# Optimization experiments

Measured on AMD Instinct MI355X. Metric: run time of the kernel, lower is better.

The kernel has to match this reference:

```python
import jax, jax.numpy as jnp
import numpy as np


def setup_inputs() -> dict:
    key = jax.random.key(0)
    k1, k2, k3, k4 = jax.random.split(key, 4)
    H = W = D = 192
    I = jax.random.normal(k1, (1, 1, H, W, D), dtype=jnp.float32)
    dx_t = jax.random.normal(k2, (1, H, W, D), dtype=jnp.float32)
    dy_t = jax.random.normal(k3, (1, H, W, D), dtype=jnp.float32)
    dz_t = jax.random.normal(k4, (1, H, W, D), dtype=jnp.float32)
    return {"I": I, "dx_t": dx_t, "dy_t": dy_t, "dz_t": dz_t}


def reference(I, dx_t, dy_t, dz_t):
    # Trilinear warp, faithful to the torch module (valid for batch=1).
    B, C, H, W, D = I.shape
    # Identity meshgrid: x varies along width (axis 1), y along height (axis 0),
    # z along depth (axis 2) -- matches the numpy construction in __init__.
    x_mesh = jnp.arange(W, dtype=jnp.float32)[None, :, None]
    y_mesh = jnp.arange(H, dtype=jnp.float32)[:, None, None]
    z_mesh = jnp.arange(D, dtype=jnp.float32)[None, None, :]
    # +1 accounts for the zero-padding of I by 1 voxel on every side.
    x = dx_t[0] + x_mesh + 1.0  # [H,W,D]
    y = dy_t[0] + y_mesh + 1.0
    z = dz_t[0] + z_mesh + 1.0

    Ip = jnp.pad(I[0], ((0, 0), (1, 1), (1, 1), (1, 1)))  # [C,H+2,W+2,D+2]
    Hp, Wp, Dp = H + 2, W + 2, D + 2

    fx = jnp.floor(x).astype(jnp.int32)
    fy = jnp.floor(y).astype(jnp.int32)
    fz = jnp.floor(z).astype(jnp.int32)
    x0 = jnp.clip(fx, 0, Wp - 1); x1 = jnp.clip(fx + 1, 0, Wp - 1)
    y0 = jnp.clip(fy, 0, Hp - 1); y1 = jnp.clip(fy + 1, 0, Hp - 1)
    z0 = jnp.clip(fz, 0, Dp - 1); z1 = jnp.clip(fz + 1, 0, Dp - 1)

    # Fractional weights computed from the *clamped* upper corner (faithful).
    dx = x1.astype(jnp.float32) - x
    dy = y1.astype(jnp.float32) - y
    dz = z1.astype(jnp.float32) - z

    # Gather 8 corners: padded volume layout is [C, y, x, z].
    Ia = Ip[:, y0, x0, z0]
    Ib = Ip[:, y1, x0, z0]
    Ic = Ip[:, y0, x1, z0]
    Id = Ip[:, y1, x1, z0]
    Ie = Ip[:, y0, x0, z1]
    If = Ip[:, y1, x0, z1]
    Ig = Ip[:, y0, x1, z1]
    Ih = Ip[:, y1, x1, z1]

    wa = dz * dx * dy
    wb = dz * dx * (1 - dy)
    wc = dz * (1 - dx) * dy
    wd = dz * (1 - dx) * (1 - dy)
    we = (1 - dz) * dx * dy
    wf = (1 - dz) * dx * (1 - dy)
    wg = (1 - dz) * (1 - dx) * dy
    wh = (1 - dz) * (1 - dx) * (1 - dy)

    out = (wa * Ia + wb * Ib + wc * Ic + wd * Id
           + we * Ie + wf * If + wg * Ig + wh * Ih)  # [C,H,W,D]
    return out[None]  # [1,C,H,W,D]
```

## Files before the change

### kernel.cpp

```cpp
#include <hip/hip_runtime.h>

constexpr int H = 192, W = 192, D = 192;
constexpr int BH = 8, BW = 8, BZ = 16;
constexpr int TY = 16, TX = 16, TZ = 24;
constexpr int WD = W * D;

__device__ __forceinline__ float ref_voxel(const float* __restrict__ I,
                                           float x, float y, float zf)
{
    int fx = (int)floorf(x), fy = (int)floorf(y), fz = (int)floorf(zf);
    int x0 = min(max(fx, 0), W + 1), x1 = min(max(fx + 1, 0), W + 1);
    int y0 = min(max(fy, 0), H + 1), y1 = min(max(fy + 1, 0), H + 1);
    int zp0 = min(max(fz, 0), D + 1), zp1 = min(max(fz + 1, 0), D + 1);
    float dx = (float)x1 - x, dy = (float)y1 - y, dz = (float)zp1 - zf;
    int xi0 = x0 - 1, xi1 = x1 - 1, yi0 = y0 - 1, yi1 = y1 - 1;
    int zi = zp0 - 1, zj = zp1 - 1;
    float ax0 = ((unsigned)xi0 < (unsigned)W) ? dx       : 0.f;
    float ax1 = ((unsigned)xi1 < (unsigned)W) ? 1.f - dx : 0.f;
    float ay0 = ((unsigned)yi0 < (unsigned)H) ? dy       : 0.f;
    float ay1 = ((unsigned)yi1 < (unsigned)H) ? 1.f - dy : 0.f;
    float az0 = ((unsigned)zi  < (unsigned)D) ? dz       : 0.f;
    float az1 = ((unsigned)zj  < (unsigned)D) ? 1.f - dz : 0.f;
    int xc0 = min(max(xi0, 0), W - 1), xc1 = min(max(xi1, 0), W - 1);
    int yc0 = min(max(yi0, 0), H - 1), yc1 = min(max(yi1, 0), H - 1);
    int zc0 = min(max(zi, 0), D - 1),  zc1 = min(max(zj, 0), D - 1);
    const float* r00 = I + (yc0 * W + xc0) * D;
    const float* r01 = I + (yc0 * W + xc1) * D;
    const float* r10 = I + (yc1 * W + xc0) * D;
    const float* r11 = I + (yc1 * W + xc1) * D;
    float s00 = az0 * r00[zc0] + az1 * r00[zc1];
    float s01 = az0 * r01[zc0] + az1 * r01[zc1];
    float s10 = az0 * r10[zc0] + az1 * r10[zc1];
    float s11 = az0 * r11[zc0] + az1 * r11[zc1];
    return ay0 * (ax0 * s00 + ax1 * s01) + ay1 * (ax0 * s10 + ax1 * s11);
}

__global__ __launch_bounds__(256) void st_tile(
    const float* __restrict__ I,
    const float* __restrict__ dxt,
    const float* __restrict__ dyt,
    const float* __restrict__ dzt,
    float* __restrict__ out)
{
    __shared__ float tile[TY * TX * TZ];

    const int tid = threadIdx.x;
    const int bx = blockIdx.x, by = blockIdx.y, bz = blockIdx.z;
    const int w0 = bx * BW, h0 = by * BH, z0 = bz * BZ;
    const int xg0 = w0 - 4, yg0 = h0 - 4, zg0 = z0 - 4;

    const int zq = tid & 3, wl = (tid >> 2) & 7, hl = tid >> 5;
    const int h = h0 + hl, w = w0 + wl, z = z0 + zq * 4;
    const int t4 = (h * W + w) * (D / 4) + (z >> 2);

    float4 vx = reinterpret_cast<const float4*>(dxt)[t4];
    float4 vy = reinterpret_cast<const float4*>(dyt)[t4];
    float4 vz = reinterpret_cast<const float4*>(dzt)[t4];

    const bool interior = (bx >= 1) & (bx <= 22) & (by >= 1) & (by <= 22)
                        & (bz >= 1) & (bz <= 10);

    float rxj[4] = {vx.x, vx.y, vx.z, vx.w};
    float ryj[4] = {vy.x, vy.y, vy.z, vy.w};
    float rzj[4] = {vz.x, vz.y, vz.z, vz.w};
    float ro[4];

    if (interior) {
        {
            const float* p0 = I + ((yg0 * W + xg0) * D + zg0);
            float4 vals[6];
            #pragma unroll
            for (int it = 0; it < 6; ++it) {
                int g = it * 256 + tid;
                int row = g / 6, c = g - row * 6;
                int ry = row >> 4, rx = row & 15;
                vals[it] = *reinterpret_cast<const float4*>(p0 + (ry * W + rx) * D + c * 4);
            }
            #pragma unroll
            for (int it = 0; it < 6; ++it) {
                *reinterpret_cast<float4*>(
                    reinterpret_cast<char*>(tile) + (size_t)(it * 4096 + tid * 16)) = vals[it];
            }
        }
        __syncthreads();

        #pragma unroll
        for (int j = 0; j < 4; ++j) {
            float ux = rxj[j] + (float)(wl + 4);
            float uy = ryj[j] + (float)(hl + 4);
            float uz = rzj[j] + (float)(zq * 4 + j + 4);

            float fxf = floorf(ux), fyf = floorf(uy), fzf = floorf(uz);
            int lx0 = (int)fxf, ly0 = (int)fyf, lz0 = (int)fzf;
            float tx = ux - fxf, ty = uy - fyf, tz = uz - fzf;

            bool ok = ((unsigned)lx0 <= (unsigned)(TX - 2))
                    & ((unsigned)ly0 <= (unsigned)(TY - 2))
                    & ((unsigned)lz0 <= (unsigned)(TZ - 2));

            if (__builtin_expect(ok, 1)) {
                int base = (ly0 * TX + lx0) * TZ + lz0;
                float a0 = tile[base],        a1 = tile[base + 1];
                float b0 = tile[base + TZ],   b1 = tile[base + TZ + 1];
                float c0 = tile[base + TX*TZ],     c1 = tile[base + TX*TZ + 1];
                float d0 = tile[base + TX*TZ+TZ],  d1 = tile[base + TX*TZ+TZ + 1];
                float wz0 = 1.f - tz, wz1 = tz;
                float wx0 = 1.f - tx, wx1 = tx;
                float wy0 = 1.f - ty, wy1 = ty;
                float s00 = wz0 * a0 + wz1 * a1;
                float s01 = wz0 * b0 + wz1 * b1;
                float s10 = wz0 * c0 + wz1 * c1;
                float s11 = wz0 * d0 + wz1 * d1;
                ro[j] = wy0 * (wx0 * s00 + wx1 * s01) + wy1 * (wx0 * s10 + wx1 * s11);
            } else {
                float x = rxj[j] + (float)(w + 1);
                float y = ryj[j] + (float)(h + 1);
                float zf = rzj[j] + (float)(z + j + 1);
                ro[j] = ref_voxel(I, x, y, zf);
            }
        }
    } else {
        {
            float4 vals[6];
            #pragma unroll
            for (int it = 0; it < 6; ++it) {
                int g = it * 256 + tid;
                int row = g / 6, c = g - row * 6;
                int ry = row >> 4, rx = row & 15;
                int gy = min(max(yg0 + ry, 0), H - 1);
                int gx = min(max(xg0 + rx, 0), W - 1);
                const float* rp = I + (gy * W + gx) * D;
                int zb = zg0 + c * 4;
                vals[it] = make_float4(rp[min(max(zb + 0, 0), D - 1)],
                                       rp[min(max(zb + 1, 0), D - 1)],
                                       rp[min(max(zb + 2, 0), D - 1)],
                                       rp[min(max(zb + 3, 0), D - 1)]);
            }
            #pragma unroll
            for (int it = 0; it < 6; ++it) {
                *reinterpret_cast<float4*>(
                    reinterpret_cast<char*>(tile) + (size_t)(it * 4096 + tid * 16)) = vals[it];
            }
        }
        __syncthreads();

        #pragma unroll
        for (int j = 0; j < 4; ++j) {
            float x = rxj[j] + (float)(w + 1);
            float y = ryj[j] + (float)(h + 1);
            float zf = rzj[j] + (float)(z + j + 1);

            int fx = (int)floorf(x), fy = (int)floorf(y), fz = (int)floorf(zf);
            int x0 = min(max(fx, 0), W + 1), x1 = min(max(fx + 1, 0), W + 1);
            int y0 = min(max(fy, 0), H + 1), y1 = min(max(fy + 1, 0), H + 1);
            int zp0 = min(max(fz, 0), D + 1), zp1 = min(max(fz + 1, 0), D + 1);

            float dx = (float)x1 - x, dy = (float)y1 - y, dz = (float)zp1 - zf;

            int xi0 = x0 - 1, xi1 = x1 - 1, yi0 = y0 - 1, yi1 = y1 - 1;
            int zi = zp0 - 1, zj2 = zp1 - 1;

            float ax0 = ((unsigned)xi0 < (unsigned)W) ? dx       : 0.f;
            float ax1 = ((unsigned)xi1 < (unsigned)W) ? 1.f - dx : 0.f;
            float ay0 = ((unsigned)yi0 < (unsigned)H) ? dy       : 0.f;
            float ay1 = ((unsigned)yi1 < (unsigned)H) ? 1.f - dy : 0.f;
            float az0 = ((unsigned)zi  < (unsigned)D) ? dz       : 0.f;
            float az1 = ((unsigned)zj2 < (unsigned)D) ? 1.f - dz : 0.f;

            int xc0 = min(max(xi0, 0), W - 1), xc1 = min(max(xi1, 0), W - 1);
            int yc0 = min(max(yi0, 0), H - 1), yc1 = min(max(yi1, 0), H - 1);
            int zc  = min(max(zi, 0), D - 2);

            bool zlo = (zi <= D - 2);
            bool zhi = (zi >= 0);

            int lx0 = xc0 - xg0, lx1 = xc1 - xg0;
            int ly0 = yc0 - yg0, ly1 = yc1 - yg0;
            int lz  = zc - zg0;

            bool ok = ((unsigned)lx0 <= (unsigned)(TX - 1))
                    & ((unsigned)lx1 <= (unsigned)(TX - 1))
                    & ((unsigned)ly0 <= (unsigned)(TY - 1))
                    & ((unsigned)ly1 <= (unsigned)(TY - 1))
                    & ((unsigned)lz  <= (unsigned)(TZ - 2));

            if (__builtin_expect(ok, 1)) {
                int b00 = (ly0 * TX + lx0) * TZ + lz;
                int b01 = (ly0 * TX + lx1) * TZ + lz;
                int b10 = (ly1 * TX + lx0) * TZ + lz;
                int b11 = (ly1 * TX + lx1) * TZ + lz;
                float a0 = tile[b00], a1 = tile[b00 + 1];
                float b0 = tile[b01], b1 = tile[b01 + 1];
                float c0 = tile[b10], c1 = tile[b10 + 1];
                float d0 = tile[b11], d1 = tile[b11 + 1];
                float v000 = zlo ? a0 : a1, v001 = zhi ? a1 : a0;
                float v010 = zlo ? b0 : b1, v011 = zhi ? b1 : b0;
                float v100 = zlo ? c0 : c1, v101 = zhi ? c1 : c0;
                float v110 = zlo ? d0 : d1, v111 = zhi ? d1 : d0;
                float s00 = az0 * v000 + az1 * v001;
                float s01 = az0 * v010 + az1 * v011;
                float s10 = az0 * v100 + az1 * v101;
                float s11 = az0 * v110 + az1 * v111;
                ro[j] = ay0 * (ax0 * s00 + ax1 * s01)
                      + ay1 * (ax0 * s10 + ax1 * s11);
            } else {
                ro[j] = ref_voxel(I, x, y, zf);
            }
        }
    }

    reinterpret_cast<float4*>(out)[t4] = make_float4(ro[0], ro[1], ro[2], ro[3]);
}

extern "C" void kernel_launch(void* const* d_in, const int* in_sizes, int n_in,
                              void* d_out, int out_size, void* d_ws, size_t ws_size,
                              hipStream_t stream) {
    const float* I   = (const float*)d_in[0];
    const float* dxt = (const float*)d_in[1];
    const float* dyt = (const float*)d_in[2];
    const float* dzt = (const float*)d_in[3];
    float* out = (float*)d_out;

    dim3 grid(W / BW, H / BH, D / BZ);
    hipLaunchKernelGGL(st_tile, grid, dim3(256), 0, stream,
                       I, dxt, dyt, dzt, out);
}
```

Measured before the change: 53.85 us.

## Enlarge warp tiles and stage the volume via direct global-to-LDS loads

Each block now covers a 16x16x16 output region with a 24x24x24 shared tile and 512 threads, with each thread producing two rows. This shrinks the halo overhead per output voxel. The tile is filled with global_load_lds builtins that write directly into LDS, using clamped coordinates. The separate interior and boundary paths are merged into one clamped, mostly branchless path. The cost is a larger shared-memory footprint per block, which may limit the number of resident blocks, plus extra clamp and select arithmetic on interior voxels.

New measurement: 48.94 us. 1.1x faster.

```diff
diff --git a/kernel.cpp b/kernel.cpp
--- a/kernel.cpp
+++ b/kernel.cpp
@@ -1,9 +1,10 @@
 #include <hip/hip_runtime.h>
 
 constexpr int H = 192, W = 192, D = 192;
-constexpr int BH = 8, BW = 8, BZ = 16;
-constexpr int TY = 16, TX = 16, TZ = 24;
-constexpr int WD = W * D;
+constexpr int BH = 16, BW = 16, BZ = 16;
+constexpr int TY = 24, TX = 24, TZ = 24;
+constexpr int TILE_N = TY * TX * TZ;
+constexpr int NINSTR = TILE_N / 4 / 64;
 
 __device__ __forceinline__ float ref_voxel(const float* __restrict__ I,
                                            float x, float y, float zf)
@@ -35,120 +36,68 @@
     return ay0 * (ax0 * s00 + ax1 * s01) + ay1 * (ax0 * s10 + ax1 * s11);
 }
 
-__global__ __launch_bounds__(256) void st_tile(
+__global__ __launch_bounds__(512) void st_tile(
     const float* __restrict__ I,
     const float* __restrict__ dxt,
     const float* __restrict__ dyt,
     const float* __restrict__ dzt,
     float* __restrict__ out)
 {
-    __shared__ float tile[TY * TX * TZ];
+    __shared__ float tile[TILE_N];
 
     const int tid = threadIdx.x;
     const int bx = blockIdx.x, by = blockIdx.y, bz = blockIdx.z;
     const int w0 = bx * BW, h0 = by * BH, z0 = bz * BZ;
     const int xg0 = w0 - 4, yg0 = h0 - 4, zg0 = z0 - 4;
 
-    const int zq = tid & 3, wl = (tid >> 2) & 7, hl = tid >> 5;
-    const int h = h0 + hl, w = w0 + wl, z = z0 + zq * 4;
-    const int t4 = (h * W + w) * (D / 4) + (z >> 2);
+    {
+        const unsigned wv = tid >> 6, lane = tid & 63;
+        for (unsigned i = wv; i < (unsigned)NINSTR; i += 8) {
+            unsigned c = i * 64u + lane;
+            unsigned row = c / 6u;
+            unsigned s = c - row * 6u;
+            unsigned ry = row / 24u;
+            unsigned rx = row - ry * 24u;
+            int gy = min(max(yg0 + (int)ry, 0), H - 1);
+            int gx = min(max(xg0 + (int)rx, 0), W - 1);
+            int zs = min(max(zg0 + (int)(s * 4u), 0), D - 4);
+            const float* src = I + ((gy * W + gx) * D + zs);
+            __builtin_amdgcn_global_load_lds(
+                (const __attribute__((address_space(1))) void*)src,
+                (__attribute__((address_space(3))) void*)(tile + i * 256u),
+                16, 0, 0);
+        }
+    }
 
-    float4 vx = reinterpret_cast<const float4*>(dxt)[t4];
-    float4 vy = reinterpret_cast<const float4*>(dyt)[t4];
-    float4 vz = reinterpret_cast<const float4*>(dzt)[t4];
+    const int zq = tid & 3, wloc = (tid >> 2) & 15, hl0 = tid >> 6;
+    const int wg = w0 + wloc;
+    float4 vx[2], vy[2], vz[2];
+    #pragma unroll
+    for (int k = 0; k < 2; ++k) {
+        int hg = h0 + hl0 + 8 * k;
+        int t4 = (hg * W + wg) * (D / 4) + (z0 >> 2) + zq;
+        vx[k] = reinterpret_cast<const float4*>(dxt)[t4];
+        vy[k] = reinterpret_cast<const float4*>(dyt)[t4];
+        vz[k] = reinterpret_cast<const float4*>(dzt)[t4];
+    }
 
-    const bool interior = (bx >= 1) & (bx <= 22) & (by >= 1) & (by <= 22)
-                        & (bz >= 1) & (bz <= 10);
+    asm volatile("s_waitcnt vmcnt(0)" ::: "memory");
+    __syncthreads();
 
-    float rxj[4] = {vx.x, vx.y, vx.z, vx.w};
-    float ryj[4] = {vy.x, vy.y, vy.z, vy.w};
-    float rzj[4] = {vz.x, vz.y, vz.z, vz.w};
-    float ro[4];
-
-    if (interior) {
-        {
-            const float* p0 = I + ((yg0 * W + xg0) * D + zg0);
-            float4 vals[6];
-            #pragma unroll
-            for (int it = 0; it < 6; ++it) {
-                int g = it * 256 + tid;
-                int row = g / 6, c = g - row * 6;
-                int ry = row >> 4, rx = row & 15;
-                vals[it] = *reinterpret_cast<const float4*>(p0 + (ry * W + rx) * D + c * 4);
-            }
-            #pragma unroll
-            for (int it = 0; it < 6; ++it) {
-                *reinterpret_cast<float4*>(
-                    reinterpret_cast<char*>(tile) + (size_t)(it * 4096 + tid * 16)) = vals[it];
-            }
-        }
-        __syncthreads();
+    float ro[2][4];
+    #pragma unroll
+    for (int k = 0; k < 2; ++k) {
+        const int hg = h0 + hl0 + 8 * k;
+        float rxj[4] = {vx[k].x, vx[k].y, vx[k].z, vx[k].w};
+        float ryj[4] = {vy[k].x, vy[k].y, vy[k].z, vy[k].w};
+        float rzj[4] = {vz[k].x, vz[k].y, vz[k].z, vz[k].w};
 
         #pragma unroll
         for (int j = 0; j < 4; ++j) {
-            float ux = rxj[j] + (float)(wl + 4);
-            float uy = ryj[j] + (float)(hl + 4);
-            float uz = rzj[j] + (float)(zq * 4 + j + 4);
-
-            float fxf = floorf(ux), fyf = floorf(uy), fzf = floorf(uz);
-            int lx0 = (int)fxf, ly0 = (int)fyf, lz0 = (int)fzf;
-            float tx = ux - fxf, ty = uy - fyf, tz = uz - fzf;
-
-            bool ok = ((unsigned)lx0 <= (unsigned)(TX - 2))
-                    & ((unsigned)ly0 <= (unsigned)(TY - 2))
-                    & ((unsigned)lz0 <= (unsigned)(TZ - 2));
-
-            if (__builtin_expect(ok, 1)) {
-                int base = (ly0 * TX + lx0) * TZ + lz0;
-                float a0 = tile[base],        a1 = tile[base + 1];
-                float b0 = tile[base + TZ],   b1 = tile[base + TZ + 1];
-                float c0 = tile[base + TX*TZ],     c1 = tile[base + TX*TZ + 1];
-                float d0 = tile[base + TX*TZ+TZ],  d1 = tile[base + TX*TZ+TZ + 1];
-                float wz0 = 1.f - tz, wz1 = tz;
-                float wx0 = 1.f - tx, wx1 = tx;
-                float wy0 = 1.f - ty, wy1 = ty;
-                float s00 = wz0 * a0 + wz1 * a1;
-                float s01 = wz0 * b0 + wz1 * b1;
-                float s10 = wz0 * c0 + wz1 * c1;
-                float s11 = wz0 * d0 + wz1 * d1;
-                ro[j] = wy0 * (wx0 * s00 + wx1 * s01) + wy1 * (wx0 * s10 + wx1 * s11);
-            } else {
-                float x = rxj[j] + (float)(w + 1);
-                float y = ryj[j] + (float)(h + 1);
-                float zf = rzj[j] + (float)(z + j + 1);
-                ro[j] = ref_voxel(I, x, y, zf);
-            }
-        }
-    } else {
-        {
-            float4 vals[6];
-            #pragma unroll
-            for (int it = 0; it < 6; ++it) {
-                int g = it * 256 + tid;
-                int row = g / 6, c = g - row * 6;
-                int ry = row >> 4, rx = row & 15;
-                int gy = min(max(yg0 + ry, 0), H - 1);
-                int gx = min(max(xg0 + rx, 0), W - 1);
-                const float* rp = I + (gy * W + gx) * D;
-                int zb = zg0 + c * 4;
-                vals[it] = make_float4(rp[min(max(zb + 0, 0), D - 1)],
-                                       rp[min(max(zb + 1, 0), D - 1)],
-                                       rp[min(max(zb + 2, 0), D - 1)],
-                                       rp[min(max(zb + 3, 0), D - 1)]);
-            }
-            #pragma unroll
-            for (int it = 0; it < 6; ++it) {
-                *reinterpret_cast<float4*>(
-                    reinterpret_cast<char*>(tile) + (size_t)(it * 4096 + tid * 16)) = vals[it];
-            }
-        }
-        __syncthreads();
-
-        #pragma unroll
-        for (int j = 0; j < 4; ++j) {
-            float x = rxj[j] + (float)(w + 1);
-            float y = ryj[j] + (float)(h + 1);
-            float zf = rzj[j] + (float)(z + j + 1);
+            const int zv = z0 + zq * 4 + j;
+            float x  = rxj[j] + (float)(wg + 1);
+            float y  = ryj[j] + (float)(hg + 1);
+            float zf = rzj[j] + (float)(zv + 1);
 
             int fx = (int)floorf(x), fy = (int)floorf(y), fz = (int)floorf(zf);
             int x0 = min(max(fx, 0), W + 1), x1 = min(max(fx + 1, 0), W + 1);
@@ -184,32 +133,38 @@
                     & ((unsigned)ly1 <= (unsigned)(TY - 1))
                     & ((unsigned)lz  <= (unsigned)(TZ - 2));
 
-            if (__builtin_expect(ok, 1)) {
-                int b00 = (ly0 * TX + lx0) * TZ + lz;
-                int b01 = (ly0 * TX + lx1) * TZ + lz;
-                int b10 = (ly1 * TX + lx0) * TZ + lz;
-                int b11 = (ly1 * TX + lx1) * TZ + lz;
-                float a0 = tile[b00], a1 = tile[b00 + 1];
-                float b0 = tile[b01], b1 = tile[b01 + 1];
-                float c0 = tile[b10], c1 = tile[b10 + 1];
-                float d0 = tile[b11], d1 = tile[b11 + 1];
-                float v000 = zlo ? a0 : a1, v001 = zhi ? a1 : a0;
-                float v010 = zlo ? b0 : b1, v011 = zhi ? b1 : b0;
-                float v100 = zlo ? c0 : c1, v101 = zhi ? c1 : c0;
-                float v110 = zlo ? d0 : d1, v111 = zhi ? d1 : d0;
-                float s00 = az0 * v000 + az1 * v001;
-                float s01 = az0 * v010 + az1 * v011;
-                float s10 = az0 * v100 + az1 * v101;
-                float s11 = az0 * v110 + az1 * v111;
-                ro[j] = ay0 * (ax0 * s00 + ax1 * s01)
-                      + ay1 * (ax0 * s10 + ax1 * s11);
-            } else {
-                ro[j] = ref_voxel(I, x, y, zf);
-            }
+            int b00 = min(max((ly0 * TX + lx0) * TZ + lz, 0), TILE_N - 2);
+            int b01 = min(max((ly0 * TX + lx1) * TZ + lz, 0), TILE_N - 2);
+            int b10 = min(max((ly1 * TX + lx0) * TZ + lz, 0), TILE_N - 2);
+            int b11 = min(max((ly1 * TX + lx1) * TZ + lz, 0), TILE_N - 2);
+
+            float a0 = tile[b00], a1 = tile[b00 + 1];
+            float b0 = tile[b01], b1 = tile[b01 + 1];
+            float c0 = tile[b10], c1 = tile[b10 + 1];
+            float d0 = tile[b11], d1 = tile[b11 + 1];
+
+            float v000 = zlo ? a0 : a1, v001 = zhi ? a1 : a0;
+            float v010 = zlo ? b0 : b1, v011 = zhi ? b1 : b0;
+            float v100 = zlo ? c0 : c1, v101 = zhi ? c1 : c0;
+            float v110 = zlo ? d0 : d1, v111 = zhi ? d1 : d0;
+            float s00 = az0 * v000 + az1 * v001;
+            float s01 = az0 * v010 + az1 * v011;
+            float s10 = az0 * v100 + az1 * v101;
+            float s11 = az0 * v110 + az1 * v111;
+            float r = ay0 * (ax0 * s00 + ax1 * s01)
+                    + ay1 * (ax0 * s10 + ax1 * s11);
+
+            ro[k][j] = __builtin_expect(ok, 1) ? r : ref_voxel(I, x, y, zf);
         }
     }
 
-    reinterpret_cast<float4*>(out)[t4] = make_float4(ro[0], ro[1], ro[2], ro[3]);
+    #pragma unroll
+    for (int k = 0; k < 2; ++k) {
+        int hg = h0 + hl0 + 8 * k;
+        int t4 = (hg * W + wg) * (D / 4) + (z0 >> 2) + zq;
+        reinterpret_cast<float4*>(out)[t4] =
+            make_float4(ro[k][0], ro[k][1], ro[k][2], ro[k][3]);
+    }
 }
 
 extern "C" void kernel_launch(void* const* d_in, const int* in_sizes, int n_in,
@@ -222,6 +177,6 @@
     float* out = (float*)d_out;
 
     dim3 grid(W / BW, H / BH, D / BZ);
-    hipLaunchKernelGGL(st_tile, grid, dim3(256), 0, stream,
+    hipLaunchKernelGGL(st_tile, grid, dim3(512), 0, stream,
                        I, dxt, dyt, dzt, out);
 }
```
